# Kernel tuning notes

Hardware: AMD Instinct MI355X
Metric: run time of the kernel (lower is better)

## Reference

```python
import jax, jax.numpy as jnp
import numpy as np

DIMS = (2000, 500, 400)
H, DK, DV = 8, 32, 32
DM = H * DV  # 256
NUM_CLASS = 5
BS = 16384
TEMP = DK ** 0.5
LN_EPS = 1e-6


def setup_inputs() -> dict:
    key = jax.random.key(0)
    ks = jax.random.split(key, 32)
    inp = {"input_data": jax.random.normal(ks[0], (BS, sum(DIMS)), dtype=jnp.float32)}
    i = 1
    for name, odim in (("q", H * DK), ("k", H * DK), ("v", H * DV)):
        for m, d in enumerate(DIMS):
            inp[f"w{name}{m}"] = jax.random.normal(ks[i], (d, odim), dtype=jnp.float32) * (1.0 / np.sqrt(d)); i += 1
            inp[f"b{name}{m}"] = jnp.zeros((odim,), dtype=jnp.float32)
    inp["fc_w"] = jax.random.normal(ks[i], (DM, DM), dtype=jnp.float32) * (1.0 / np.sqrt(DM)); i += 1
    inp["fc_b"] = jnp.zeros((DM,), dtype=jnp.float32)
    inp["ln_g"] = jnp.ones((DM,), dtype=jnp.float32)
    inp["ln_b"] = jnp.zeros((DM,), dtype=jnp.float32)
    inp["out_w"] = jax.random.normal(ks[i], (len(DIMS) * DM, NUM_CLASS), dtype=jnp.float32) * (1.0 / np.sqrt(len(DIMS) * DM)); i += 1
    inp["out_b"] = jnp.zeros((NUM_CLASS,), dtype=jnp.float32)
    return inp


def _forward(input_data, wq, bq, wk, bk, wv, bv, fc_w, fc_b, ln_g, ln_b, out_w, out_b):
    bs = input_data.shape[0]
    M = len(DIMS)
    offs = np.concatenate([[0], np.cumsum(DIMS)])
    xs = [input_data[:, offs[m]:offs[m + 1]] for m in range(M)]
    # per-modality projections -> [bs, M, H*D]
    q = jnp.stack([xs[m] @ wq[m] + bq[m] for m in range(M)], axis=1)
    k = jnp.stack([xs[m] @ wk[m] + bk[m] for m in range(M)], axis=1)
    v = jnp.stack([xs[m] @ wv[m] + bv[m] for m in range(M)], axis=1)
    # [bs, H, M, D]
    qh = q.reshape(bs, M, H, DK).transpose(0, 2, 1, 3)
    kh = k.reshape(bs, M, H, DK).transpose(0, 2, 1, 3)
    vh = v.reshape(bs, M, H, DV).transpose(0, 2, 1, 3)
    attn = jnp.einsum("bhmd,bhnd->bhmn", qh / TEMP, kh)
    attn = attn / jnp.abs(attn.min())  # global-min scaling as in source
    attn = attn / jnp.maximum(jnp.sum(jnp.abs(attn), axis=-1, keepdims=True), 1e-12)  # L1 normalize
    attn = jax.nn.softmax(attn, axis=-1)
    o = jnp.einsum("bhmn,bhnd->bhmd", attn, vh)
    o = o.transpose(0, 2, 1, 3).reshape(bs, M, DM)
    residual = v  # [bs, M, DM]
    o = o @ fc_w + fc_b
    x = o + residual
    mu = x.mean(axis=-1, keepdims=True)
    var = ((x - mu) ** 2).mean(axis=-1, keepdims=True)
    x = (x - mu) / jnp.sqrt(var + LN_EPS) * ln_g + ln_b
    return x.reshape(bs, -1) @ out_w + out_b


def reference(input_data, wq0, bq0, wq1, bq1, wq2, bq2, wk0, bk0, wk1, bk1, wk2, bk2,
              wv0, bv0, wv1, bv1, wv2, bv2, fc_w, fc_b, ln_g, ln_b, out_w, out_b):
    return _forward(input_data, (wq0, wq1, wq2), (bq0, bq1, bq2), (wk0, wk1, wk2), (bk0, bk1, bk2),
                    (wv0, wv1, wv2), (bv0, bv1, bv2), fc_w, fc_b, ln_g, ln_b, out_w, out_b)
```

## Files before the change

### kernel.cpp

```cpp
#include <hip/hip_runtime.h>
#include <hip/hip_bf16.h>

#define BATCH 16384
#define HEADS 8
#define DDK 32
#define NQKV 768
#define NCLASS 5
#define LN_EPS 1e-6f

#define BM 128
#define BN 128
#define BKK 32

typedef _Float16 f16x8 __attribute__((ext_vector_type(8)));
typedef float f32x4 __attribute__((ext_vector_type(4)));

__device__ __forceinline__ void gl16(const void* g, void* l) {
    __builtin_amdgcn_global_load_lds(
        (const __attribute__((address_space(1))) unsigned int*)g,
        (__attribute__((address_space(3))) unsigned int*)l, 16, 0, 0);
}

struct WArgs {
    const float* w[3][3];
    const float* b[3][3];
    const float* fcw;
    _Float16* Bt;
    float* biasx;
    _Float16* fcWh;
};

__global__ __launch_bounds__(256) void convert_w_all(WArgs a) {
    const int y = blockIdx.y;
    const int gid = blockIdx.x * 256 + threadIdx.x;
    if (y < 3) {
        const int m = y;
        const int Kdim = (m == 0) ? 2000 : (m == 1 ? 500 : 400);
        const int Kpad = (m == 0) ? 2048 : 512;
        if (gid < NQKV) {
            const int p = gid >> 8, c = gid & 255;
            a.biasx[m * NQKV + gid] = a.b[p][m][c];
        }
        _Float16* dst0 = a.Bt;
        if (m >= 1) dst0 += (size_t)NQKV * 2048;
        if (m == 2) dst0 += (size_t)NQKV * 512;
        const int k8n = Kpad >> 3;
        const int total = NQKV * k8n;
        for (int i = gid; i < total; i += gridDim.x * 256) {
            const int kb = i / NQKV;
            const int n = i - kb * NQKV;
            const int k8 = kb << 3;
            const int p = n >> 8, c = n & 255;
            const float* wsrc = a.w[p][m];
            union { _Float16 h[8]; uint4 v; } hi;
#pragma unroll
            for (int j = 0; j < 8; ++j) {
                float x = (k8 + j < Kdim) ? wsrc[(size_t)(k8 + j) * 256 + c] : 0.f;
                hi.h[j] = (_Float16)x;
            }
            *reinterpret_cast<uint4*>(dst0 + (size_t)n * Kpad + k8) = hi.v;
        }
    } else {
        for (int i = gid; i < 256 * 32; i += gridDim.x * 256) {
            const int n = i & 255;
            const int k8 = (i >> 8) << 3;
            union { _Float16 h[8]; uint4 v; } hi;
#pragma unroll
            for (int j = 0; j < 8; ++j)
                hi.h[j] = (_Float16)a.fcw[(size_t)(k8 + j) * 256 + n];
            *reinterpret_cast<uint4*>(a.fcWh + (size_t)n * 256 + k8) = hi.v;
        }
    }
}

struct GemmArgs {
    const float* X;
    const _Float16* B[3];
    int ldB[3];
    int nk[3];
    int Kd[3];
    int xoff[3];
};

struct Aregs { float4 v[4]; };

__device__ __forceinline__ void loadA(const float* xbase, int k0, int Kd, int kh,
                                      Aregs& R) {
    if (k0 + 32 <= Kd) {
#pragma unroll
        for (int j = 0; j < 4; ++j)
            R.v[j] = *reinterpret_cast<const float4*>(xbase + k0 + j * 4);
    } else {
#pragma unroll
        for (int j = 0; j < 4; ++j) {
            float4 t = make_float4(0.f, 0.f, 0.f, 0.f);
            const int kb = k0 + kh + j * 4;
            if (kb + 0 < Kd) t.x = xbase[k0 + j * 4 + 0];
            if (kb + 1 < Kd) t.y = xbase[k0 + j * 4 + 1];
            if (kb + 2 < Kd) t.z = xbase[k0 + j * 4 + 2];
            if (kb + 3 < Kd) t.w = xbase[k0 + j * 4 + 3];
            R.v[j] = t;
        }
    }
}

__device__ __forceinline__ void cvtSplit(const Aregs& R, uint4& h0, uint4& h1,
                                         uint4& l0, uint4& l1) {
    union { _Float16 h[8]; uint4 v; } H0, H1, L0, L1;
    float f[16];
#pragma unroll
    for (int j = 0; j < 4; ++j) {
        f[j * 4 + 0] = R.v[j].x; f[j * 4 + 1] = R.v[j].y;
        f[j * 4 + 2] = R.v[j].z; f[j * 4 + 3] = R.v[j].w;
    }
#pragma unroll
    for (int e = 0; e < 8; ++e) {
        _Float16 h = (_Float16)f[e];
        H0.h[e] = h;
        L0.h[e] = (_Float16)(f[e] - (float)h);
    }
#pragma unroll
    for (int e = 0; e < 8; ++e) {
        _Float16 h = (_Float16)f[8 + e];
        H1.h[e] = h;
        L1.h[e] = (_Float16)(f[8 + e] - (float)h);
    }
    h0 = H0.v; h1 = H1.v; l0 = L0.v; l1 = L1.v;
}

__global__ __launch_bounds__(256) void qkv_mfma_all(
    GemmArgs ga, const float* __restrict__ biasx,
    float* __restrict__ Qo, float* __restrict__ Ko, float* __restrict__ Vo) {
    const int z = blockIdx.z;
    const _Float16* __restrict__ Bt = ga.B[z];
    const int ldB = ga.ldB[z];
    const int nkz = ga.nk[z];
    const int Kd = ga.Kd[z];
    const float* __restrict__ bias = biasx + z * NQKV;

    const int row0l = blockIdx.x * BM;
    const int nb = blockIdx.y * BN;
    const int tid = threadIdx.x;
    const int lane = tid & 63;
    const int w = tid >> 6;
    const int wr = w >> 1, wc = w & 1;

    __shared__ alignas(16) _Float16 AsH[BM * BKK];
    __shared__ alignas(16) _Float16 AsL[BM * BKK];
    __shared__ alignas(16) _Float16 Bs[BN * BKK];

    f32x4 acc[4][4];
#pragma unroll
    for (int i = 0; i < 4; ++i)
#pragma unroll
        for (int j = 0; j < 4; ++j) acc[i][j] = (f32x4){0.f, 0.f, 0.f, 0.f};

    const int ar = tid >> 1;
    const int kh = (tid & 1) * 16;
    const float* xbase = ga.X + (size_t)(row0l + ar) * 2900 + ga.xoff[z] + kh;
    uint4* wrH = reinterpret_cast<uint4*>(&AsH[tid * 16]);
    uint4* wrL = reinterpret_cast<uint4*>(&AsL[tid * 16]);

    const int rs = lane >> 2;
    const int kkv = (lane & 3) * 8;
    const size_t gB0 = (size_t)(nb + w * 16 + rs) * ldB + kkv;
    const size_t gB1 = (size_t)(nb + (w + 4) * 16 + rs) * ldB + kkv;
    _Float16* lB0 = &Bs[(w * 16) * BKK];
    _Float16* lB1 = &Bs[((w + 4) * 16) * BKK];

    const int fr = lane & 15;
    const int fk = (lane >> 4) * 8;
    const int aoff0 = (wr * 64 + fr) * BKK + fk;
    const int boff0 = (wc * 64 + fr) * BKK + fk;

    Aregs RA, RB;
    uint4 pAh0, pAh1, pAl0, pAl1;
    uint4 pBh0, pBh1, pBl0, pBl1;

    loadA(xbase, 0, Kd, kh, RA);
    cvtSplit(RA, pAh0, pAh1, pAl0, pAl1);

#pragma unroll 1
    for (int kt = 0; kt < nkz; kt += 2) {
        {
            const int k0 = kt * BKK;
            __syncthreads();
            wrH[0] = pAh0; wrH[1] = pAh1;
            wrL[0] = pAl0; wrL[1] = pAl1;
            gl16(Bt + gB0 + k0, lB0);
            gl16(Bt + gB1 + k0, lB1);
            __syncthreads();
            loadA(xbase, (kt + 1) * BKK, Kd, kh, RB);
            f16x8 b[4];
#pragma unroll
            for (int ni = 0; ni < 4; ++ni)
                b[ni] = *reinterpret_cast<const f16x8*>(&Bs[boff0 + ni * 16 * BKK]);
            f16x8 a[4];
#pragma unroll
            for (int mi = 0; mi < 4; ++mi)
                a[mi] = *reinterpret_cast<const f16x8*>(&AsH[aoff0 + mi * 16 * BKK]);
#pragma unroll
            for (int mi = 0; mi < 4; ++mi)
#pragma unroll
                for (int ni = 0; ni < 4; ++ni)
                    acc[mi][ni] = __builtin_amdgcn_mfma_f32_16x16x32_f16(
                        a[mi], b[ni], acc[mi][ni], 0, 0, 0);
#pragma unroll
            for (int mi = 0; mi < 4; ++mi)
                a[mi] = *reinterpret_cast<const f16x8*>(&AsL[aoff0 + mi * 16 * BKK]);
#pragma unroll
            for (int mi = 0; mi < 4; ++mi)
#pragma unroll
                for (int ni = 0; ni < 4; ++ni)
                    acc[mi][ni] = __builtin_amdgcn_mfma_f32_16x16x32_f16(
                        a[mi], b[ni], acc[mi][ni], 0, 0, 0);
            cvtSplit(RB, pBh0, pBh1, pBl0, pBl1);
        }
        {
            const int k0 = (kt + 1) * BKK;
            __syncthreads();
            wrH[0] = pBh0; wrH[1] = pBh1;
            wrL[0] = pBl0; wrL[1] = pBl1;
            gl16(Bt + gB0 + k0, lB0);
            gl16(Bt + gB1 + k0, lB1);
            __syncthreads();
            if (kt + 2 < nkz) loadA(xbase, (kt + 2) * BKK, Kd, kh, RA);
            f16x8 b[4];
#pragma unroll
            for (int ni = 0; ni < 4; ++ni)
                b[ni] = *reinterpret_cast<const f16x8*>(&Bs[boff0 + ni * 16 * BKK]);
            f16x8 a[4];
#pragma unroll
            for (int mi = 0; mi < 4; ++mi)
                a[mi] = *reinterpret_cast<const f16x8*>(&AsH[aoff0 + mi * 16 * BKK]);
#pragma unroll
            for (int mi = 0; mi < 4; ++mi)
#pragma unroll
                for (int ni = 0; ni < 4; ++ni)
                    acc[mi][ni] = __builtin_amdgcn_mfma_f32_16x16x32_f16(
                        a[mi], b[ni], acc[mi][ni], 0, 0, 0);
#pragma unroll
            for (int mi = 0; mi < 4; ++mi)
                a[mi] = *reinterpret_cast<const f16x8*>(&AsL[aoff0 + mi * 16 * BKK]);
#pragma unroll
            for (int mi = 0; mi < 4; ++mi)
#pragma unroll
                for (int ni = 0; ni < 4; ++ni)
                    acc[mi][ni] = __builtin_amdgcn_mfma_f32_16x16x32_f16(
                        a[mi], b[ni], acc[mi][ni], 0, 0, 0);
            cvtSplit(RA, pAh0, pAh1, pAl0, pAl1);
        }
    }

#pragma unroll
    for (int ni = 0; ni < 4; ++ni) {
        const int gc = nb + wc * 64 + ni * 16 + fr;
        const int proj = gc >> 8;
        const int col = gc & 255;
        const float bv = bias[gc];
        float* outp = (proj == 0 ? Qo : proj == 1 ? Ko : Vo);
#pragma unroll
        for (int mi = 0; mi < 4; ++mi) {
            const int gr = row0l + wr * 64 + mi * 16 + (lane >> 4) * 4;
            float* p = outp + (size_t)gr * NQKV + z * 256 + col;
#pragma unroll
            for (int j = 0; j < 4; ++j)
                p[(size_t)j * NQKV] = acc[mi][ni][j] + bv;
        }
    }
}

__global__ __launch_bounds__(256) void attn_kernel(const float* __restrict__ Q,
                                                   const float* __restrict__ K,
                                                   const float* __restrict__ V,
                                                   _Float16* __restrict__ Of) {
    const int s = blockIdx.x;
    const int t = threadIdx.x;
    __shared__ float qs[NQKV], ks[NQKV], vs[NQKV];
    __shared__ float att[HEADS][3][3];

    const size_t base = (size_t)s * NQKV;
    for (int i = t; i < NQKV; i += 256) {
        qs[i] = Q[base + i];
        ks[i] = K[base + i];
        vs[i] = V[base + i];
    }
    __syncthreads();

    if (t < 72) {
        const int h = t / 9, ij = t % 9, i = ij / 3, j = ij % 3;
        const float* qp = &qs[i * 256 + h * 32];
        const float* kp = &ks[j * 256 + h * 32];
        float sc = 0.f;
#pragma unroll
        for (int d = 0; d < DDK; ++d) sc = fmaf(qp[d], kp[d], sc);
        att[h][i][j] = sc;
    }
    __syncthreads();
    if (t < 24) {
        const int h = t / 3, i = t % 3;
        float s0 = att[h][i][0], s1 = att[h][i][1], s2 = att[h][i][2];
        float r = fabsf(s0) + fabsf(s1) + fabsf(s2);
        r = fmaxf(r, 1e-12f);
        float p0 = s0 / r, p1 = s1 / r, p2 = s2 / r;
        float mx = fmaxf(p0, fmaxf(p1, p2));
        float e0 = expf(p0 - mx), e1 = expf(p1 - mx), e2 = expf(p2 - mx);
        float inv = 1.f / (e0 + e1 + e2);
        att[h][i][0] = e0 * inv;
        att[h][i][1] = e1 * inv;
        att[h][i][2] = e2 * inv;
    }
    __syncthreads();

    const int c = t;
    const int h = c >> 5;
#pragma unroll
    for (int m = 0; m < 3; ++m) {
        float o = att[h][m][0] * vs[c] + att[h][m][1] * vs[256 + c] + att[h][m][2] * vs[512 + c];
        const size_t ob = ((size_t)s * 3 + m) * 512 + c;
        _Float16 oh = (_Float16)o;
        Of[ob] = oh;
        Of[ob + 256] = (_Float16)(o - (float)oh);
    }
}

__global__ __launch_bounds__(256) void fc_mfma(const _Float16* __restrict__ O,
                                               const _Float16* __restrict__ Wh,
                                               const float* __restrict__ fcb,
                                               const float* __restrict__ resid,
                                               float* __restrict__ X) {
    const int row0 = blockIdx.x * BM;
    const int nb = blockIdx.y * BN;
    const int tid = threadIdx.x;
    const int lane = tid & 63;
    const int w = tid >> 6;
    const int wr = w >> 1, wc = w & 1;

    __shared__ alignas(16) _Float16 AsH[BM * BKK];
    __shared__ alignas(16) _Float16 AsL[BM * BKK];
    __shared__ alignas(16) _Float16 BsH[BN * BKK];

    f32x4 acc[4][4];
#pragma unroll
    for (int i = 0; i < 4; ++i)
#pragma unroll
        for (int j = 0; j < 4; ++j) acc[i][j] = (f32x4){0.f, 0.f, 0.f, 0.f};

    const int rs = lane >> 2;
    const int kk = (lane & 3) * 8;
    const size_t gA0 = (size_t)(row0 + w * 16 + rs) * 512 + kk;
    const size_t gA1 = (size_t)(row0 + (w + 4) * 16 + rs) * 512 + kk;
    const size_t gB0 = (size_t)(nb + w * 16 + rs) * 256 + kk;
    const size_t gB1 = (size_t)(nb + (w + 4) * 16 + rs) * 256 + kk;
    _Float16* lAH0 = &AsH[w * 512];
    _Float16* lAH1 = &AsH[(w + 4) * 512];
    _Float16* lAL0 = &AsL[w * 512];
    _Float16* lAL1 = &AsL[(w + 4) * 512];
    _Float16* lBH0 = &BsH[w * 512];
    _Float16* lBH1 = &BsH[(w + 4) * 512];

    const int fr = lane & 15;
    const int fk = (lane >> 4) * 8;
    const int aoff0 = (wr * 64 + fr) * BKK + fk;
    const int boff0 = (wc * 64 + fr) * BKK + fk;

#pragma unroll 1
    for (int kt = 0; kt < 8; ++kt) {
        const int k0 = kt * BKK;
        __syncthreads();
        gl16(O + gA0 + k0, lAH0);
        gl16(O + gA1 + k0, lAH1);
        gl16(O + 256 + gA0 + k0, lAL0);
        gl16(O + 256 + gA1 + k0, lAL1);
        gl16(Wh + gB0 + k0, lBH0);
        gl16(Wh + gB1 + k0, lBH1);
        __syncthreads();

        f16x8 ah[4], bh[4];
#pragma unroll
        for (int mi = 0; mi < 4; ++mi)
            ah[mi] = *reinterpret_cast<const f16x8*>(&AsH[aoff0 + mi * 16 * BKK]);
#pragma unroll
        for (int ni = 0; ni < 4; ++ni)
            bh[ni] = *reinterpret_cast<const f16x8*>(&BsH[boff0 + ni * 16 * BKK]);
#pragma unroll
        for (int mi = 0; mi < 4; ++mi)
#pragma unroll
            for (int ni = 0; ni < 4; ++ni)
                acc[mi][ni] = __builtin_amdgcn_mfma_f32_16x16x32_f16(
                    ah[mi], bh[ni], acc[mi][ni], 0, 0, 0);
        {
            f16x8 al[4];
#pragma unroll
            for (int mi = 0; mi < 4; ++mi)
                al[mi] = *reinterpret_cast<const f16x8*>(&AsL[aoff0 + mi * 16 * BKK]);
#pragma unroll
            for (int mi = 0; mi < 4; ++mi)
#pragma unroll
                for (int ni = 0; ni < 4; ++ni)
                    acc[mi][ni] = __builtin_amdgcn_mfma_f32_16x16x32_f16(
                        al[mi], bh[ni], acc[mi][ni], 0, 0, 0);
        }
    }

#pragma unroll
    for (int ni = 0; ni < 4; ++ni) {
        const int gc = nb + wc * 64 + ni * 16 + fr;
        const float bv = fcb[gc];
#pragma unroll
        for (int mi = 0; mi < 4; ++mi) {
            const int gr = row0 + wr * 64 + mi * 16 + (lane >> 4) * 4;
#pragma unroll
            for (int j = 0; j < 4; ++j) {
                const size_t off = (size_t)(gr + j) * 256 + gc;
                X[off] = acc[mi][ni][j] + bv + resid[off];
            }
        }
    }
}

__global__ __launch_bounds__(256) void ln_out_kernel(const float* __restrict__ X,
                                                     const float* __restrict__ g,
                                                     const float* __restrict__ bb,
                                                     const float* __restrict__ ow,
                                                     const float* __restrict__ ob,
                                                     float* __restrict__ out) {
    const int s = blockIdx.x;
    const int t = threadIdx.x;
    const int lane = t & 63, wv = t >> 6;
    __shared__ float xr[NQKV];
    __shared__ float red1[4], red2[4];
    __shared__ float cpart[4][NCLASS];

    const size_t base = (size_t)s * NQKV;
    const float gg = g[t];
    const float bbv = bb[t];

    for (int m = 0; m < 3; ++m) {
        float v = X[base + m * 256 + t];
        float s1 = v, s2 = v * v;
#pragma unroll
        for (int off = 32; off > 0; off >>= 1) {
            s1 += __shfl_down(s1, off);
            s2 += __shfl_down(s2, off);
        }
        if (lane == 0) { red1[wv] = s1; red2[wv] = s2; }
        __syncthreads();
        const float tot = red1[0] + red1[1] + red1[2] + red1[3];
        const float tot2 = red2[0] + red2[1] + red2[2] + red2[3];
        const float mu = tot * (1.f / 256.f);
        const float var = tot2 * (1.f / 256.f) - mu * mu;
        const float inv = 1.0f / sqrtf(var + LN_EPS);
        xr[m * 256 + t] = (v - mu) * inv * gg + bbv;
        __syncthreads();
    }

    float p[NCLASS] = {0.f, 0.f, 0.f, 0.f, 0.f};
    for (int i = t; i < NQKV; i += 256) {
        const float xv = xr[i];
#pragma unroll
        for (int c = 0; c < NCLASS; ++c) p[c] = fmaf(xv, ow[i * NCLASS + c], p[c]);
    }
#pragma unroll
    for (int c = 0; c < NCLASS; ++c) {
        float pv = p[c];
#pragma unroll
        for (int off = 32; off > 0; off >>= 1) pv += __shfl_down(pv, off);
        if (lane == 0) cpart[wv][c] = pv;
    }
    __syncthreads();
    if (t < NCLASS)
        out[(size_t)s * NCLASS + t] =
            cpart[0][t] + cpart[1][t] + cpart[2][t] + cpart[3][t] + ob[t];
}

extern "C" void kernel_launch(void* const* d_in, const int* in_sizes, int n_in,
                              void* d_out, int out_size, void* d_ws, size_t ws_size,
                              hipStream_t stream) {
    const float* x = (const float*)d_in[0];
    WArgs wa;
    int idx = 1;
    for (int p = 0; p < 3; ++p)
        for (int m = 0; m < 3; ++m) {
            wa.w[p][m] = (const float*)d_in[idx++];
            wa.b[p][m] = (const float*)d_in[idx++];
        }
    const float* fc_w = (const float*)d_in[19];
    const float* fc_b = (const float*)d_in[20];
    const float* ln_g = (const float*)d_in[21];
    const float* ln_b = (const float*)d_in[22];
    const float* out_w = (const float*)d_in[23];
    const float* out_b = (const float*)d_in[24];

    float* ws = (float*)d_ws;
    const size_t SZ = (size_t)BATCH * NQKV;
    float* Q = ws;
    float* Kb = ws + SZ;
    float* Vb = ws + 2 * SZ;
    float* biasx = ws + 3 * SZ;
    _Float16* Bt = (_Float16*)(biasx + 3 * NQKV);
    _Float16* fcWh = Bt + (size_t)NQKV * 3072;
    _Float16* Of = fcWh + 256 * 256;

    wa.fcw = fc_w; wa.Bt = Bt; wa.biasx = biasx; wa.fcWh = fcWh;

    float* X = Q;

    convert_w_all<<<dim3(768, 4), 256, 0, stream>>>(wa);

    GemmArgs ga;
    ga.X = x;
    ga.B[0] = Bt;
    ga.B[1] = Bt + (size_t)NQKV * 2048;
    ga.B[2] = Bt + (size_t)NQKV * 2048 + (size_t)NQKV * 512;
    ga.ldB[0] = 2048; ga.ldB[1] = 512; ga.ldB[2] = 512;
    ga.nk[0] = 64; ga.nk[1] = 16; ga.nk[2] = 14;
    ga.Kd[0] = 2000; ga.Kd[1] = 500; ga.Kd[2] = 400;
    ga.xoff[0] = 0; ga.xoff[1] = 2000; ga.xoff[2] = 2500;

    dim3 g(BATCH / BM, NQKV / BN, 3);
    qkv_mfma_all<<<g, 256, 0, stream>>>(ga, biasx, Q, Kb, Vb);

    attn_kernel<<<BATCH, 256, 0, stream>>>(Q, Kb, Vb, Of);

    fc_mfma<<<dim3((BATCH * 3) / BM, 2), 256, 0, stream>>>(Of, fcWh, fc_b, Vb, X);

    ln_out_kernel<<<BATCH, 256, 0, stream>>>(X, ln_g, ln_b, out_w, out_b, (float*)d_out);
}
```

Baseline: 654.9 us.

## Fuse attention, fc projection, layernorm and output head into one kernel

```diff
diff --git a/kernel.cpp b/kernel.cpp
--- a/kernel.cpp
+++ b/kernel.cpp
@@ -270,208 +270,186 @@
     }
 }
 
-__global__ __launch_bounds__(256) void attn_kernel(const float* __restrict__ Q,
-                                                   const float* __restrict__ K,
-                                                   const float* __restrict__ V,
-                                                   _Float16* __restrict__ Of) {
-    const int s = blockIdx.x;
+__global__ __launch_bounds__(256) void attn_fc_ln_out(
+    const float* __restrict__ Q, const float* __restrict__ K,
+    const float* __restrict__ V, const _Float16* __restrict__ Wh,
+    const float* __restrict__ fcb, const float* __restrict__ lng,
+    const float* __restrict__ lnb, const float* __restrict__ ow,
+    const float* __restrict__ ob, float* __restrict__ out) {
+    const int s0 = blockIdx.x * 4;
     const int t = threadIdx.x;
-    __shared__ float qs[NQKV], ks[NQKV], vs[NQKV];
-    __shared__ float att[HEADS][3][3];
-
-    const size_t base = (size_t)s * NQKV;
-    for (int i = t; i < NQKV; i += 256) {
-        qs[i] = Q[base + i];
-        ks[i] = K[base + i];
-        vs[i] = V[base + i];
-    }
-    __syncthreads();
-
-    if (t < 72) {
-        const int h = t / 9, ij = t % 9, i = ij / 3, j = ij % 3;
-        const float* qp = &qs[i * 256 + h * 32];
-        const float* kp = &ks[j * 256 + h * 32];
+    const int lane = t & 63;
+    const int w = t >> 6;
+
+    __shared__ alignas(16) float QK[6656];
+    __shared__ float Vs[3072];
+    __shared__ float att[288];
+    __shared__ float mu_s[16], inv_s[16];
+
+    const size_t qb = (size_t)s0 * NQKV;
+    for (int i = t; i < 3072; i += 256) {
+        QK[i]        = Q[qb + i];
+        QK[3072 + i] = K[qb + i];
+        Vs[i]        = V[qb + i];
+    }
+    __syncthreads();
+
+    for (int i = t; i < 288; i += 256) {
+        const int s = i / 72;
+        const int e = i - s * 72;
+        const int h = e / 9;
+        const int e9 = e - h * 9;
+        const int qi = e9 / 3;
+        const int kj = e9 - qi * 3;
+        const float* qp = &QK[s * NQKV + qi * 256 + h * 32];
+        const float* kp = &QK[3072 + s * NQKV + kj * 256 + h * 32];
         float sc = 0.f;
 #pragma unroll
         for (int d = 0; d < DDK; ++d) sc = fmaf(qp[d], kp[d], sc);
-        att[h][i][j] = sc;
-    }
-    __syncthreads();
-    if (t < 24) {
-        const int h = t / 3, i = t % 3;
-        float s0 = att[h][i][0], s1 = att[h][i][1], s2 = att[h][i][2];
-        float r = fabsf(s0) + fabsf(s1) + fabsf(s2);
+        att[i] = sc;
+    }
+    __syncthreads();
+
+    if (t < 96) {
+        const int s = t / 24;
+        const int e = t - s * 24;
+        const int h = e / 3;
+        const int qi = e - h * 3;
+        float* ap = &att[s * 72 + h * 9 + qi * 3];
+        float s0v = ap[0], s1v = ap[1], s2v = ap[2];
+        float r = fabsf(s0v) + fabsf(s1v) + fabsf(s2v);
         r = fmaxf(r, 1e-12f);
-        float p0 = s0 / r, p1 = s1 / r, p2 = s2 / r;
+        float p0 = s0v / r, p1 = s1v / r, p2 = s2v / r;
         float mx = fmaxf(p0, fmaxf(p1, p2));
         float e0 = expf(p0 - mx), e1 = expf(p1 - mx), e2 = expf(p2 - mx);
         float inv = 1.f / (e0 + e1 + e2);
-        att[h][i][0] = e0 * inv;
-        att[h][i][1] = e1 * inv;
-        att[h][i][2] = e2 * inv;
-    }
-    __syncthreads();
-
-    const int c = t;
-    const int h = c >> 5;
-#pragma unroll
-    for (int m = 0; m < 3; ++m) {
-        float o = att[h][m][0] * vs[c] + att[h][m][1] * vs[256 + c] + att[h][m][2] * vs[512 + c];
-        const size_t ob = ((size_t)s * 3 + m) * 512 + c;
-        _Float16 oh = (_Float16)o;
-        Of[ob] = oh;
-        Of[ob + 256] = (_Float16)(o - (float)oh);
-    }
-}
-
-__global__ __launch_bounds__(256) void fc_mfma(const _Float16* __restrict__ O,
-                                               const _Float16* __restrict__ Wh,
-                                               const float* __restrict__ fcb,
-                                               const float* __restrict__ resid,
-                                               float* __restrict__ X) {
-    const int row0 = blockIdx.x * BM;
-    const int nb = blockIdx.y * BN;
-    const int tid = threadIdx.x;
-    const int lane = tid & 63;
-    const int w = tid >> 6;
-    const int wr = w >> 1, wc = w & 1;
-
-    __shared__ alignas(16) _Float16 AsH[BM * BKK];
-    __shared__ alignas(16) _Float16 AsL[BM * BKK];
-    __shared__ alignas(16) _Float16 BsH[BN * BKK];
-
-    f32x4 acc[4][4];
-#pragma unroll
-    for (int i = 0; i < 4; ++i)
-#pragma unroll
-        for (int j = 0; j < 4; ++j) acc[i][j] = (f32x4){0.f, 0.f, 0.f, 0.f};
-
-    const int rs = lane >> 2;
-    const int kk = (lane & 3) * 8;
-    const size_t gA0 = (size_t)(row0 + w * 16 + rs) * 512 + kk;
-    const size_t gA1 = (size_t)(row0 + (w + 4) * 16 + rs) * 512 + kk;
-    const size_t gB0 = (size_t)(nb + w * 16 + rs) * 256 + kk;
-    const size_t gB1 = (size_t)(nb + (w + 4) * 16 + rs) * 256 + kk;
-    _Float16* lAH0 = &AsH[w * 512];
-    _Float16* lAH1 = &AsH[(w + 4) * 512];
-    _Float16* lAL0 = &AsL[w * 512];
-    _Float16* lAL1 = &AsL[(w + 4) * 512];
-    _Float16* lBH0 = &BsH[w * 512];
-    _Float16* lBH1 = &BsH[(w + 4) * 512];
-
+        ap[0] = e0 * inv; ap[1] = e1 * inv; ap[2] = e2 * inv;
+    }
+    __syncthreads();
+
+    {
+        char* OhiB = reinterpret_cast<char*>(&QK[0]);
+        char* OloB = reinterpret_cast<char*>(&QK[2048]);
+        const int c = t;
+        const int h = c >> 5;
+#pragma unroll
+        for (int ra = 0; ra < 16; ++ra) {
+            float o = 0.f;
+            if (ra < 12) {
+                const int s = ra / 3, m = ra - (ra / 3) * 3;
+                const float* ap = &att[s * 72 + h * 9 + m * 3];
+                o = ap[0] * Vs[s * NQKV + c] + ap[1] * Vs[s * NQKV + 256 + c] +
+                    ap[2] * Vs[s * NQKV + 512 + c];
+            }
+            _Float16 oh = (_Float16)o;
+            _Float16 ol = (_Float16)(o - (float)oh);
+            const int bo = (ra * 512 + c * 2) ^ ((ra & 7) << 4);
+            *reinterpret_cast<_Float16*>(OhiB + bo) = oh;
+            *reinterpret_cast<_Float16*>(OloB + bo) = ol;
+        }
+    }
+    __syncthreads();
+
+    f32x4 acc[4];
+#pragma unroll
+    for (int nb = 0; nb < 4; ++nb) acc[nb] = (f32x4){0.f, 0.f, 0.f, 0.f};
     const int fr = lane & 15;
     const int fk = (lane >> 4) * 8;
-    const int aoff0 = (wr * 64 + fr) * BKK + fk;
-    const int boff0 = (wc * 64 + fr) * BKK + fk;
-
-#pragma unroll 1
-    for (int kt = 0; kt < 8; ++kt) {
-        const int k0 = kt * BKK;
-        __syncthreads();
-        gl16(O + gA0 + k0, lAH0);
-        gl16(O + gA1 + k0, lAH1);
-        gl16(O + 256 + gA0 + k0, lAL0);
-        gl16(O + 256 + gA1 + k0, lAL1);
-        gl16(Wh + gB0 + k0, lBH0);
-        gl16(Wh + gB1 + k0, lBH1);
-        __syncthreads();
-
-        f16x8 ah[4], bh[4];
-#pragma unroll
-        for (int mi = 0; mi < 4; ++mi)
-            ah[mi] = *reinterpret_cast<const f16x8*>(&AsH[aoff0 + mi * 16 * BKK]);
-#pragma unroll
-        for (int ni = 0; ni < 4; ++ni)
-            bh[ni] = *reinterpret_cast<const f16x8*>(&BsH[boff0 + ni * 16 * BKK]);
-#pragma unroll
-        for (int mi = 0; mi < 4; ++mi)
-#pragma unroll
-            for (int ni = 0; ni < 4; ++ni)
-                acc[mi][ni] = __builtin_amdgcn_mfma_f32_16x16x32_f16(
-                    ah[mi], bh[ni], acc[mi][ni], 0, 0, 0);
-        {
-            f16x8 al[4];
-#pragma unroll
-            for (int mi = 0; mi < 4; ++mi)
-                al[mi] = *reinterpret_cast<const f16x8*>(&AsL[aoff0 + mi * 16 * BKK]);
-#pragma unroll
-            for (int mi = 0; mi < 4; ++mi)
-#pragma unroll
-                for (int ni = 0; ni < 4; ++ni)
-                    acc[mi][ni] = __builtin_amdgcn_mfma_f32_16x16x32_f16(
-                        al[mi], bh[ni], acc[mi][ni], 0, 0, 0);
-        }
-    }
-
-#pragma unroll
-    for (int ni = 0; ni < 4; ++ni) {
-        const int gc = nb + wc * 64 + ni * 16 + fr;
-        const float bv = fcb[gc];
-#pragma unroll
-        for (int mi = 0; mi < 4; ++mi) {
-            const int gr = row0 + wr * 64 + mi * 16 + (lane >> 4) * 4;
+    {
+        const char* OhiB = reinterpret_cast<const char*>(&QK[0]);
+        const char* OloB = reinterpret_cast<const char*>(&QK[2048]);
+#pragma unroll
+        for (int ks = 0; ks < 8; ++ks) {
+            const int abo = (fr * 512 + (ks * 32 + fk) * 2) ^ ((fr & 7) << 4);
+            f16x8 ah = *reinterpret_cast<const f16x8*>(OhiB + abo);
+            f16x8 al = *reinterpret_cast<const f16x8*>(OloB + abo);
+#pragma unroll
+            for (int nb = 0; nb < 4; ++nb) {
+                const _Float16* bp =
+                    &Wh[(size_t)(w * 64 + nb * 16 + fr) * 256 + ks * 32 + fk];
+                f16x8 b = *reinterpret_cast<const f16x8*>(bp);
+                acc[nb] = __builtin_amdgcn_mfma_f32_16x16x32_f16(ah, b, acc[nb], 0, 0, 0);
+                acc[nb] = __builtin_amdgcn_mfma_f32_16x16x32_f16(al, b, acc[nb], 0, 0, 0);
+            }
+        }
+    }
+    __syncthreads();
+
+    {
+        float* Xs = &QK[0];
+#pragma unroll
+        for (int nb = 0; nb < 4; ++nb) {
+            const int col = w * 64 + nb * 16 + fr;
+            const float bv = fcb[col];
 #pragma unroll
             for (int j = 0; j < 4; ++j) {
-                const size_t off = (size_t)(gr + j) * 256 + gc;
-                X[off] = acc[mi][ni][j] + bv + resid[off];
-            }
-        }
-    }
-}
-
-__global__ __launch_bounds__(256) void ln_out_kernel(const float* __restrict__ X,
-                                                     const float* __restrict__ g,
-                                                     const float* __restrict__ bb,
-                                                     const float* __restrict__ ow,
-                                                     const float* __restrict__ ob,
-                                                     float* __restrict__ out) {
-    const int s = blockIdx.x;
-    const int t = threadIdx.x;
-    const int lane = t & 63, wv = t >> 6;
-    __shared__ float xr[NQKV];
-    __shared__ float red1[4], red2[4];
-    __shared__ float cpart[4][NCLASS];
-
-    const size_t base = (size_t)s * NQKV;
-    const float gg = g[t];
-    const float bbv = bb[t];
-
-    for (int m = 0; m < 3; ++m) {
-        float v = X[base + m * 256 + t];
-        float s1 = v, s2 = v * v;
-#pragma unroll
-        for (int off = 32; off > 0; off >>= 1) {
-            s1 += __shfl_down(s1, off);
-            s2 += __shfl_down(s2, off);
-        }
-        if (lane == 0) { red1[wv] = s1; red2[wv] = s2; }
-        __syncthreads();
-        const float tot = red1[0] + red1[1] + red1[2] + red1[3];
-        const float tot2 = red2[0] + red2[1] + red2[2] + red2[3];
-        const float mu = tot * (1.f / 256.f);
-        const float var = tot2 * (1.f / 256.f) - mu * mu;
-        const float inv = 1.0f / sqrtf(var + LN_EPS);
-        xr[m * 256 + t] = (v - mu) * inv * gg + bbv;
-        __syncthreads();
-    }
-
-    float p[NCLASS] = {0.f, 0.f, 0.f, 0.f, 0.f};
-    for (int i = t; i < NQKV; i += 256) {
-        const float xv = xr[i];
-#pragma unroll
-        for (int c = 0; c < NCLASS; ++c) p[c] = fmaf(xv, ow[i * NCLASS + c], p[c]);
-    }
-#pragma unroll
-    for (int c = 0; c < NCLASS; ++c) {
-        float pv = p[c];
-#pragma unroll
-        for (int off = 32; off > 0; off >>= 1) pv += __shfl_down(pv, off);
-        if (lane == 0) cpart[wv][c] = pv;
-    }
-    __syncthreads();
-    if (t < NCLASS)
-        out[(size_t)s * NCLASS + t] =
-            cpart[0][t] + cpart[1][t] + cpart[2][t] + cpart[3][t] + ob[t];
+                const int row = (lane >> 4) * 4 + j;
+                if (row < 12) {
+                    const int s = row / 3, m = row - (row / 3) * 3;
+                    const float xn =
+                        acc[nb][j] + bv + Vs[s * NQKV + m * 256 + col];
+                    Xs[row * 260 + col] = xn;
+                }
+            }
+        }
+    }
+    __syncthreads();
+
+    {
+        const float* Xs = &QK[0];
+#pragma unroll
+        for (int rr = 0; rr < 3; ++rr) {
+            const int row = w * 3 + rr;
+            float s1 = 0.f, s2 = 0.f;
+#pragma unroll
+            for (int kk = 0; kk < 4; ++kk) {
+                const float v = Xs[row * 260 + lane + kk * 64];
+                s1 += v; s2 += v * v;
+            }
+#pragma unroll
+            for (int off = 32; off > 0; off >>= 1) {
+                s1 += __shfl_down(s1, off);
+                s2 += __shfl_down(s2, off);
+            }
+            if (lane == 0) {
+                const float mu = s1 * (1.f / 256.f);
+                const float var = s2 * (1.f / 256.f) - mu * mu;
+                mu_s[row] = mu;
+                inv_s[row] = 1.0f / sqrtf(var + LN_EPS);
+            }
+        }
+    }
+    __syncthreads();
+
+    {
+        const float* Xs = &QK[0];
+        const int si = w;
+        float p[NCLASS] = {0.f, 0.f, 0.f, 0.f, 0.f};
+#pragma unroll
+        for (int m = 0; m < 3; ++m) {
+            const int row = si * 3 + m;
+            const float mu = mu_s[row], inv = inv_s[row];
+#pragma unroll
+            for (int kk = 0; kk < 4; ++kk) {
+                const int col = lane + kk * 64;
+                const float xr =
+                    (Xs[row * 260 + col] - mu) * inv * lng[col] + lnb[col];
+                const float* owp = &ow[(size_t)(m * 256 + col) * NCLASS];
+#pragma unroll
+                for (int c = 0; c < NCLASS; ++c) p[c] = fmaf(xr, owp[c], p[c]);
+            }
+        }
+#pragma unroll
+        for (int c = 0; c < NCLASS; ++c) {
+#pragma unroll
+            for (int off = 32; off > 0; off >>= 1) p[c] += __shfl_down(p[c], off);
+        }
+        if (lane == 0) {
+#pragma unroll
+            for (int c = 0; c < NCLASS; ++c)
+                out[(size_t)(s0 + si) * NCLASS + c] = p[c] + ob[c];
+        }
+    }
 }
 
 extern "C" void kernel_launch(void* const* d_in, const int* in_sizes, int n_in,
@@ -500,11 +478,8 @@
     float* biasx = ws + 3 * SZ;
     _Float16* Bt = (_Float16*)(biasx + 3 * NQKV);
     _Float16* fcWh = Bt + (size_t)NQKV * 3072;
-    _Float16* Of = fcWh + 256 * 256;
 
     wa.fcw = fc_w; wa.Bt = Bt; wa.biasx = biasx; wa.fcWh = fcWh;
-
-    float* X = Q;
 
     convert_w_all<<<dim3(768, 4), 256, 0, stream>>>(wa);
 
@@ -521,9 +496,6 @@
     dim3 g(BATCH / BM, NQKV / BN, 3);
     qkv_mfma_all<<<g, 256, 0, stream>>>(ga, biasx, Q, Kb, Vb);
 
-    attn_kernel<<<BATCH, 256, 0, stream>>>(Q, Kb, Vb, Of);
-
-    fc_mfma<<<dim3((BATCH * 3) / BM, 2), 256, 0, stream>>>(Of, fcWh, fc_b, Vb, X);
-
-    ln_out_kernel<<<BATCH, 256, 0, stream>>>(X, ln_g, ln_b, out_w, out_b, (float*)d_out);
-}
+    attn_fc_ln_out<<<BATCH / 4, 256, 0, stream>>>(
+        Q, Kb, Vb, fcWh, fc_b, ln_g, ln_b, out_w, out_b, (float*)d_out);
+}
```

After: 645.7 us. About the same (-1.4%).
